# Kernel tuning notes

Hardware: AMD Instinct MI355X
Metric: run time of the kernel (lower is better)

## Reference

```python
import jax, jax.numpy as jnp
import numpy as np

B, S, D = 8, 2048, 2048          # batch, seq, hidden
E, K, NSTEPS = 16, 2, 4          # routed experts, top_k, routers
NSH = 2                          # shared experts
DR = D // 4                      # routed inner dim (routed_ratio=4)
DS = D // 2                      # shared inner dim (shared_ratio=2)


def setup_inputs() -> dict:
    key = jax.random.key(0)
    ks = jax.random.split(key, 8)
    s = 0.02
    return {
        "x": jax.random.normal(ks[0], (B, S, D), jnp.float32),
        "step_t": 1,
        "router_w": jax.random.normal(ks[1], (NSTEPS, D, E), jnp.float32) * s,
        "re_w1": jax.random.normal(ks[2], (E, D, DR), jnp.float32) * s,
        "re_b1": jnp.zeros((E, DR), jnp.float32),
        "re_w2": jax.random.normal(ks[3], (E, DR, D), jnp.float32) * s,
        "re_b2": jnp.zeros((E, D), jnp.float32),
        "sh_w1": jax.random.normal(ks[4], (NSH, D, DS), jnp.float32) * s,
        "sh_b1": jnp.zeros((NSH, DS), jnp.float32),
        "sh_w2": jax.random.normal(ks[5], (NSH, DS, D), jnp.float32) * s,
        "sh_b2": jnp.zeros((NSH, D), jnp.float32),
    }


def reference(x, step_t, router_w, re_w1, re_b1, re_w2, re_b2, sh_w1, sh_b1, sh_w2, sh_b2):
    orig = x.shape
    flat = x.reshape(-1, orig[-1])                       # [T, D]
    T = flat.shape[0]

    # shared expert group: sum of always-active experts
    h = jax.nn.silu(jnp.einsum('td,sdk->tsk', flat, sh_w1) + sh_b1)   # [T, NSH, DS]
    out = jnp.einsum('tsk,skd->td', h, sh_w2) + sh_b2.sum(0)          # [T, D]

    # top-k router for this step (eval mode: no jitter noise)
    logits = flat @ router_w[step_t]                     # [T, E]
    probs = jax.nn.softmax(logits, axis=-1)
    w, idx = jax.lax.top_k(probs, K)                     # [T, K]

    # combine weights per (token, expert): sum_k w_k * 1[idx_k == e]
    cw = jnp.zeros((T, E), flat.dtype).at[jnp.arange(T)[:, None], idx].add(w)

    # routed experts: masked gather-compute-scatter expressed as
    # weighted accumulation (zero combine-weight == token not routed)
    def body(acc, p):
        w1, b1, w2, b2, cwe = p                          # cwe: [T]
        ye = jax.nn.silu(flat @ w1 + b1) @ w2 + b2       # [T, D]
        return acc + cwe[:, None] * ye, None

    out, _ = jax.lax.scan(body, out, (re_w1, re_b1, re_w2, re_b2, cw.T))
    return out.reshape(orig)
```

## Files before the change

kernel.cpp:

```cpp
#include <hip/hip_runtime.h>
#include <hip/hip_bf16.h>
#include <stdint.h>


#define DEV static __device__ __forceinline__

typedef __attribute__((ext_vector_type(8))) short bf16x8;
typedef __attribute__((ext_vector_type(4))) float f32x4;

constexpr int T_TOK = 16384;
constexpr int DIM   = 2048;
constexpr int NEXP  = 16;
constexpr int DR_K  = 512;
constexpr int DS_K  = 1024;
constexpr int MAXROWS = 34816;
constexpr int MAXTILES = 272;

DEV void gload16(const void* g, void* l) {
  __builtin_amdgcn_global_load_lds(
      (const __attribute__((address_space(1))) unsigned int*)g,
      (__attribute__((address_space(3))) unsigned int*)l, 16, 0, 0);
}

DEV float silu_f(float v) { return v / (1.f + __expf(-v)); }

__global__ __launch_bounds__(256) void cast_router_kernel(
    const float* __restrict__ x, __hip_bfloat16* __restrict__ xb,
    const float* __restrict__ rw_all, const int* __restrict__ step_p,
    int* __restrict__ tk_idx, float* __restrict__ tk_w) {
  int tid = threadIdx.x;
  int t0 = blockIdx.x * 8;
  __shared__ float xs[8][1024];
  __shared__ float red[4][4][8][4];

  float acc[8][4];
#pragma unroll
  for (int tk = 0; tk < 8; ++tk)
#pragma unroll
    for (int j = 0; j < 4; ++j) acc[tk][j] = 0.f;

  const float* rwbase = rw_all + (size_t)step_p[0] * DIM * NEXP;

#pragma unroll
  for (int half = 0; half < 2; ++half) {
#pragma unroll
    for (int tk = 0; tk < 8; ++tk) {
      const float4* xp = (const float4*)(x + (size_t)(t0 + tk) * DIM + half * 1024);
      float4 v = xp[tid];
      *(float4*)&xs[tk][tid * 4] = v;
      union { ushort4 u; __hip_bfloat16 h[4]; } o;
      o.h[0] = __float2bfloat16(v.x); o.h[1] = __float2bfloat16(v.y);
      o.h[2] = __float2bfloat16(v.z); o.h[3] = __float2bfloat16(v.w);
      *(ushort4*)(xb + (size_t)(t0 + tk) * DIM + half * 1024 + tid * 4) = o.u;
    }
    __syncthreads();
    const float4* rw4 = (const float4*)(rwbase + (size_t)half * 1024 * NEXP);
#pragma unroll 4
    for (int i = 0; i < 16; ++i) {
      int c = i * 256 + tid;
      int d = c >> 2;
      float4 wv = rw4[c];
#pragma unroll
      for (int tk = 0; tk < 8; ++tk) {
        float v = xs[tk][d];
        acc[tk][0] += v * wv.x; acc[tk][1] += v * wv.y;
        acc[tk][2] += v * wv.z; acc[tk][3] += v * wv.w;
      }
    }
    __syncthreads();
  }

#pragma unroll
  for (int m = 4; m < 64; m <<= 1) {
#pragma unroll
    for (int tk = 0; tk < 8; ++tk) {
      acc[tk][0] += __shfl_xor(acc[tk][0], m);
      acc[tk][1] += __shfl_xor(acc[tk][1], m);
      acc[tk][2] += __shfl_xor(acc[tk][2], m);
      acc[tk][3] += __shfl_xor(acc[tk][3], m);
    }
  }
  int lane = tid & 63, wvi = tid >> 6;
  if (lane < 4) {
#pragma unroll
    for (int tk = 0; tk < 8; ++tk) {
      float4 r = {acc[tk][0], acc[tk][1], acc[tk][2], acc[tk][3]};
      *(float4*)&red[wvi][lane][tk][0] = r;
    }
  }
  __syncthreads();
  if (tid < 8) {
    int t = t0 + tid;
    float lg[16];
#pragma unroll
    for (int e = 0; e < 16; ++e) {
      int cg = e >> 2, j = e & 3;
      lg[e] = red[0][cg][tid][j] + red[1][cg][tid][j] +
              red[2][cg][tid][j] + red[3][cg][tid][j];
    }
    float mx = lg[0];
    for (int i = 1; i < 16; ++i) mx = fmaxf(mx, lg[i]);
    float pr[16], sum = 0.f;
    for (int i = 0; i < 16; ++i) { pr[i] = expf(lg[i] - mx); sum += pr[i]; }
    float inv = 1.f / sum;
    int b0 = -1, b1 = -1; float w0 = -1.f, w1 = -1.f;
    for (int i = 0; i < 16; ++i) {
      float v = pr[i] * inv;
      if (v > w0)      { w1 = w0; b1 = b0; w0 = v; b0 = i; }
      else if (v > w1) { w1 = v; b1 = i; }
    }
    tk_idx[2 * t] = b0; tk_idx[2 * t + 1] = b1;
    tk_w[2 * t] = w0;   tk_w[2 * t + 1] = w1;
  }
}

__global__ __launch_bounds__(256) void hist_kernel(const int* __restrict__ tk_idx,
                                                   int* __restrict__ cnt_pad) {
  __shared__ int lc[16];
  int tid = threadIdx.x;
  if (tid < 16) lc[tid] = 0;
  __syncthreads();
  int base = blockIdx.x * 2048;
#pragma unroll
  for (int i = 0; i < 8; ++i)
    atomicAdd(&lc[tk_idx[base + i * 256 + tid]], 1);
  __syncthreads();
  if (tid < 16) atomicAdd(&cnt_pad[tid * 16], lc[tid]);
}

__global__ __launch_bounds__(256) void transpose_cast(const float* __restrict__ in,
                                                      __hip_bfloat16* __restrict__ out,
                                                      int R, int C) {
  __shared__ float t[64][68];
  size_t bo = (size_t)blockIdx.z * R * C;
  in += bo; out += bo;
  int c0 = blockIdx.x * 64, r0 = blockIdx.y * 64;
  int tid = threadIdx.x;
  int rr = tid >> 2, cc0 = (tid & 3) * 16;
  const float* ip = in + (size_t)(r0 + rr) * C + c0 + cc0;
#pragma unroll
  for (int j = 0; j < 4; ++j)
    *(float4*)&t[rr][cc0 + 4 * j] = *(const float4*)(ip + 4 * j);
  __syncthreads();
  int wr = tid >> 2, wc0 = (tid & 3) * 16;
  union { bf16x8 v; __hip_bfloat16 h[8]; } o0, o1;
#pragma unroll
  for (int k = 0; k < 8; ++k) o0.h[k] = __float2bfloat16(t[wc0 + k][wr]);
#pragma unroll
  for (int k = 0; k < 8; ++k) o1.h[k] = __float2bfloat16(t[wc0 + 8 + k][wr]);
  __hip_bfloat16* op = out + (size_t)(c0 + wr) * R + r0 + wc0;
  *(bf16x8*)op = o0.v;
  *(bf16x8*)(op + 8) = o1.v;
}

__global__ void scan_kernel(const int* __restrict__ cnt_pad, int* __restrict__ seg,
                            int* __restrict__ padded, int* __restrict__ tile_e,
                            int* __restrict__ tile_m0, int* __restrict__ n_tiles) {
  if (threadIdx.x == 0) {
    int off = 0, nt = 0;
    for (int e = 0; e < NEXP; ++e) {
      seg[e] = off;
      int pc = (cnt_pad[e * 16] + 127) & ~127;
      padded[e] = pc;
      for (int m = 0; m < pc; m += 128) { tile_e[nt] = e; tile_m0[nt] = m; ++nt; }
      off += pc;
    }
    seg[NEXP] = off;
    n_tiles[0] = nt;
  }
}

__global__ __launch_bounds__(256) void scatter_kernel(
    const int* __restrict__ tk_idx, const float* __restrict__ tk_w,
    const int* __restrict__ seg, int* __restrict__ cnt2_pad,
    int* __restrict__ tok_list, float* __restrict__ w_list,
    int* __restrict__ pos_list) {
  __shared__ int lh[16], lbase[16];
  int tid = threadIdx.x;
  if (tid < 16) lh[tid] = 0;
  __syncthreads();
  int t = blockIdx.x * 256 + tid;
  int e0 = tk_idx[2 * t], e1 = tk_idx[2 * t + 1];
  int s0 = atomicAdd(&lh[e0], 1);
  int s1 = atomicAdd(&lh[e1], 1);
  __syncthreads();
  if (tid < 16) lbase[tid] = atomicAdd(&cnt2_pad[tid * 16], lh[tid]);
  __syncthreads();
  int p0 = seg[e0] + lbase[e0] + s0;
  int p1 = seg[e1] + lbase[e1] + s1;
  tok_list[p0] = t; w_list[p0] = tk_w[2 * t];     pos_list[2 * t] = p0;
  tok_list[p1] = t; w_list[p1] = tk_w[2 * t + 1]; pos_list[2 * t + 1] = p1;
}

__global__ void pad_kernel(const int* __restrict__ cnt_pad, const int* __restrict__ padded,
                           const int* __restrict__ seg, int* __restrict__ tok_list,
                           float* __restrict__ w_list) {
  int e = blockIdx.x;
  int c = cnt_pad[e * 16], pc = padded[e], s = seg[e];
  for (int i = c + threadIdx.x; i < pc; i += blockDim.x) {
    tok_list[s + i] = 0;
    w_list[s + i] = 0.f;
  }
}

DEV void swz_tile(int bid, int NB, int& tile, int& nb) {
  tile = 8 * (bid / (8 * NB)) + (bid & 7);
  nb = (bid >> 3) % NB;
}

template <int MODE>
DEV void gemm_shared(const __hip_bfloat16* __restrict__ Abase,
                     const __hip_bfloat16* __restrict__ Bt,
                     const float* __restrict__ bias,
                     __hip_bfloat16* __restrict__ outb) {
  constexpr int KD = DIM;
  constexpr int NT = KD / 64;

  int tid = threadIdx.x;
  int ln = tid & 63, w8 = tid >> 6;
  int wm = w8 >> 2, wn = w8 & 3;
  int tile, nb;
  swz_tile(blockIdx.x, 8, tile, nb);
  int m0 = tile * 256;
  int n0 = nb * 256;

  __shared__ __align__(16) char lds[2 * 65536];

  int lrow = w8 * 8 + (ln >> 3);
  int cg8 = (((ln & 7) ^ (ln >> 3)) << 3);
  int browBase;
  if constexpr (MODE == 0) {
    int s = n0 >> 10, nn = n0 & 1023;
    browBase = s * DS_K + nn;
  } else {
    browBase = n0;
  }
  const __hip_bfloat16 *aSrc[2][2], *bSrc[2][2];
  int dA[2][2], dB[2][2];
#pragma unroll
  for (int h = 0; h < 2; ++h)
#pragma unroll
    for (int l = 0; l < 2; ++l) {
      aSrc[h][l] = Abase + (size_t)(m0 + h * 128 + l * 64 + lrow) * KD + cg8;
      bSrc[h][l] = Bt + (size_t)(browBase + h * 128 + l * 64 + lrow) * KD + cg8;
      dA[h][l] = h * 16384 + (l * 8 + w8) * 1024;
      dB[h][l] = 32768 + h * 16384 + (l * 8 + w8) * 1024;
    }

#pragma unroll
  for (int h = 0; h < 2; ++h)
#pragma unroll
    for (int l = 0; l < 2; ++l) {
      gload16(aSrc[h][l], lds + dA[h][l]);
      gload16(bSrc[h][l], lds + dB[h][l]);
    }
  asm volatile("s_waitcnt vmcnt(0)" ::: "memory");
  __builtin_amdgcn_s_barrier();

  f32x4 acc[8][4];
#pragma unroll
  for (int i = 0; i < 8; ++i)
#pragma unroll
    for (int j = 0; j < 4; ++j) acc[i][j] = (f32x4){0.f, 0.f, 0.f, 0.f};

  int rbyte = (ln & 15) * 128;
  int ch0 = (((ln >> 4) ^ (ln & 7)) << 4);
  int ch1 = (((4 + (ln >> 4)) ^ (ln & 7)) << 4);
  int aBase = wm * 16384 + rbyte;
  int bBase = 32768 + wn * 8192 + rbyte;

  bf16x8 af[4][2], bfr[4][2];

  for (int t = 0; t < NT; ++t) {
    const char* buf = lds + (t & 1) * 65536;
    char* nxt = lds + ((t + 1) & 1) * 65536;
    bool pf = (t + 1) < NT;
    int ko = (t + 1) * 64;

    if (pf) {
      gload16(aSrc[0][0] + ko, nxt + dA[0][0]);
      gload16(aSrc[0][1] + ko, nxt + dA[0][1]);
    }
#pragma unroll
    for (int mf = 0; mf < 4; ++mf) {
      af[mf][0] = *(const bf16x8*)(buf + aBase + mf * 2048 + ch0);
      af[mf][1] = *(const bf16x8*)(buf + aBase + mf * 2048 + ch1);
    }
#pragma unroll
    for (int nf = 0; nf < 2; ++nf) {
      bfr[nf][0] = *(const bf16x8*)(buf + bBase + nf * 2048 + ch0);
      bfr[nf][1] = *(const bf16x8*)(buf + bBase + nf * 2048 + ch1);
    }
    __builtin_amdgcn_s_barrier();
    __builtin_amdgcn_s_setprio(1);
#pragma unroll
    for (int mf = 0; mf < 4; ++mf)
#pragma unroll
      for (int nf = 0; nf < 2; ++nf)
#pragma unroll
        for (int kk = 0; kk < 2; ++kk)
          acc[mf][nf] = __builtin_amdgcn_mfma_f32_16x16x32_bf16(
              af[mf][kk], bfr[nf][kk], acc[mf][nf], 0, 0, 0);
    __builtin_amdgcn_s_setprio(0);
    __builtin_amdgcn_s_barrier();

    if (pf) {
      gload16(aSrc[1][0] + ko, nxt + dA[1][0]);
      gload16(aSrc[1][1] + ko, nxt + dA[1][1]);
    }
#pragma unroll
    for (int nf = 2; nf < 4; ++nf) {
      bfr[nf][0] = *(const bf16x8*)(buf + bBase + nf * 2048 + ch0);
      bfr[nf][1] = *(const bf16x8*)(buf + bBase + nf * 2048 + ch1);
    }
    __builtin_amdgcn_s_barrier();
    __builtin_amdgcn_s_setprio(1);
#pragma unroll
    for (int mf = 0; mf < 4; ++mf)
#pragma unroll
      for (int nf = 2; nf < 4; ++nf)
#pragma unroll
        for (int kk = 0; kk < 2; ++kk)
          acc[mf][nf] = __builtin_amdgcn_mfma_f32_16x16x32_bf16(
              af[mf][kk], bfr[nf][kk], acc[mf][nf], 0, 0, 0);
    __builtin_amdgcn_s_setprio(0);
    __builtin_amdgcn_s_barrier();

    if (pf) {
      gload16(bSrc[0][0] + ko, nxt + dB[0][0]);
      gload16(bSrc[0][1] + ko, nxt + dB[0][1]);
    }
#pragma unroll
    for (int mf = 0; mf < 4; ++mf) {
      af[mf][0] = *(const bf16x8*)(buf + aBase + (4 + mf) * 2048 + ch0);
      af[mf][1] = *(const bf16x8*)(buf + aBase + (4 + mf) * 2048 + ch1);
    }
    __builtin_amdgcn_s_barrier();
    __builtin_amdgcn_s_setprio(1);
#pragma unroll
    for (int mf = 0; mf < 4; ++mf)
#pragma unroll
      for (int nf = 0; nf < 2; ++nf)
#pragma unroll
        for (int kk = 0; kk < 2; ++kk)
          acc[4 + mf][nf] = __builtin_amdgcn_mfma_f32_16x16x32_bf16(
              af[mf][kk], bfr[nf][kk], acc[4 + mf][nf], 0, 0, 0);
    __builtin_amdgcn_s_setprio(0);
    __builtin_amdgcn_s_barrier();

    if (pf) {
      gload16(bSrc[1][0] + ko, nxt + dB[1][0]);
      gload16(bSrc[1][1] + ko, nxt + dB[1][1]);
    }
    __builtin_amdgcn_s_setprio(1);
#pragma unroll
    for (int mf = 0; mf < 4; ++mf)
#pragma unroll
      for (int nf = 2; nf < 4; ++nf)
#pragma unroll
        for (int kk = 0; kk < 2; ++kk)
          acc[4 + mf][nf] = __builtin_amdgcn_mfma_f32_16x16x32_bf16(
              af[mf][kk], bfr[nf][kk], acc[4 + mf][nf], 0, 0, 0);
    __builtin_amdgcn_s_setprio(0);

    if (pf) {
      asm volatile("s_waitcnt vmcnt(0)" ::: "memory");
      __builtin_amdgcn_s_barrier();
    }
  }

  int colc = ln & 15;
  int rowb = (ln >> 4) << 2;
#pragma unroll
  for (int mi = 0; mi < 8; ++mi) {
    int mlb = wm * 128 + mi * 16 + rowb;
#pragma unroll
    for (int ni = 0; ni < 4; ++ni) {
      int ng = n0 + wn * 64 + ni * 16 + colc;
#pragma unroll
      for (int j = 0; j < 4; ++j) {
        float v = acc[mi][ni][j];
        if constexpr (MODE == 0) {
          float s = silu_f(v + bias[ng]);
          outb[(size_t)(m0 + mlb + j) * 2048 + ng] = __float2bfloat16(s);
        } else {
          outb[(size_t)(m0 + mlb + j) * DIM + ng] =
              __float2bfloat16(v + bias[ng] + bias[DIM + ng]);
        }
      }
    }
  }
}

template <int MODE, int NB>
DEV void gemm_routed(const __hip_bfloat16* __restrict__ Abase,
                     const __hip_bfloat16* __restrict__ Bt,
                     const float* __restrict__ bias,
                     __hip_bfloat16* __restrict__ outb,
                     const int* __restrict__ tok_list,
                     const float* __restrict__ w_list,
                     const int* __restrict__ seg_off,
                     const int* __restrict__ tile_e,
                     const int* __restrict__ tile_m0,
                     const int* __restrict__ n_tiles) {
  constexpr int KD = (MODE == 3) ? DR_K : DIM;
  constexpr int NT = KD / 32;

  int tid = threadIdx.x;
  int ln = tid & 63, w8 = tid >> 6;
  int wm = w8 >> 2, wn = w8 & 3;

  __shared__ __align__(16) char lds[3 * 24576];
  __shared__ int tk_s[128];
  __shared__ float w_s[128];

  int W = n_tiles[0] * NB;
  int q = (W + 7) >> 3;
  int xcd = blockIdx.x & 7, k = blockIdx.x >> 3;
  if (k >= q) return;
  int w = xcd * q + k;
  if (w >= W) return;
  int tl = w / NB, nb = w % NB;

  int e = tile_e[tl];
  int m0 = tile_m0[tl];
  int n0 = nb * 256;
  int seg = seg_off[e];
  if (tid < 128) {
    if constexpr (MODE == 2) tk_s[tid] = tok_list[seg + m0 + tid];
    w_s[tid] = w_list[seg + m0 + tid];
  }
  __syncthreads();

  int srow = tid >> 2;
  int schunk = (tid & 3) ^ ((tid >> 3) & 3);
  const __hip_bfloat16 *aS, *bS0, *bS1;
  {
    int ar, br0;
    if constexpr (MODE == 2) { ar = tk_s[srow]; br0 = e * DR_K + n0 + srow; }
    else                     { ar = seg + m0 + srow; br0 = e * DIM + n0 + srow; }
    aS  = Abase + (size_t)ar * KD + schunk * 8;
    bS0 = Bt + (size_t)br0 * KD + schunk * 8;
    bS1 = bS0 + (size_t)128 * KD;
  }
  int wlds = w8 * 1024;

#pragma unroll
  for (int tt = 0; tt < 2; ++tt) {
    char* sl = lds + tt * 24576;
    int ko = tt * 32;
    gload16(aS + ko, sl + wlds);
    gload16(bS0 + ko, sl + 8192 + wlds);
    gload16(bS1 + ko, sl + 16384 + wlds);
  }
  asm volatile("s_waitcnt vmcnt(3)" ::: "memory");
  __builtin_amdgcn_s_barrier();

  f32x4 acc[4][4];
#pragma unroll
  for (int i = 0; i < 4; ++i)
#pragma unroll
    for (int j = 0; j < 4; ++j) acc[i][j] = (f32x4){0.f, 0.f, 0.f, 0.f};

  int rof = (ln & 15) * 64 + ((((ln >> 4) ^ (ln >> 1)) & 3) << 4);
  int aoffs = wm * 4096 + rof;
  int boffs = 8192 + wn * 4096 + rof;

  int s0 = 0;
  for (int t = 0; t < NT; ++t) {
    const char* sl = lds + s0 * 24576;
    int sd = s0 - 1; if (sd < 0) sd += 3;
    char* dst = lds + sd * 24576;
    bool pf = (t + 2) < NT;
    int ko = (t + 2) * 32;

    if (pf) {
      gload16(aS + ko, dst + wlds);
      gload16(bS0 + ko, dst + 8192 + wlds);
      gload16(bS1 + ko, dst + 16384 + wlds);
    }
    bf16x8 af[4], bfr[4];
#pragma unroll
    for (int fi = 0; fi < 4; ++fi)
      af[fi] = *(const bf16x8*)(sl + aoffs + fi * 1024);
#pragma unroll
    for (int ni = 0; ni < 4; ++ni)
      bfr[ni] = *(const bf16x8*)(sl + boffs + ni * 1024);
    __builtin_amdgcn_s_barrier();
    __builtin_amdgcn_s_setprio(1);
#pragma unroll
    for (int fi = 0; fi < 4; ++fi)
#pragma unroll
      for (int ni = 0; ni < 4; ++ni)
        acc[fi][ni] = __builtin_amdgcn_mfma_f32_16x16x32_bf16(af[fi], bfr[ni], acc[fi][ni], 0, 0, 0);
    __builtin_amdgcn_s_setprio(0);

    if (t + 1 < NT) {
      if (pf) asm volatile("s_waitcnt vmcnt(3)" ::: "memory");
      else    asm volatile("s_waitcnt vmcnt(0)" ::: "memory");
      __builtin_amdgcn_s_barrier();
    }
    s0 = (s0 + 1 == 3) ? 0 : s0 + 1;
  }

  int colc = ln & 15;
  int rowb = (ln >> 4) << 2;
#pragma unroll
  for (int mi = 0; mi < 4; ++mi) {
    int mlb = wm * 64 + mi * 16 + rowb;
#pragma unroll
    for (int ni = 0; ni < 4; ++ni) {
      int ng = n0 + wn * 64 + ni * 16 + colc;
#pragma unroll
      for (int j = 0; j < 4; ++j) {
        float v = acc[mi][ni][j];
        int ml = mlb + j;
        if constexpr (MODE == 2) {
          float s = silu_f(v + bias[(size_t)e * DR_K + ng]) * w_s[ml];
          outb[((size_t)seg + m0 + ml) * DR_K + ng] = __float2bfloat16(s);
        } else {
          float wv = w_s[ml];
          outb[((size_t)seg + m0 + ml) * DIM + ng] =
              __float2bfloat16(v + wv * bias[(size_t)e * DIM + ng]);
        }
      }
    }
  }
}

__global__ __launch_bounds__(512) void gemm_sh_l1(
    const __hip_bfloat16* A, const __hip_bfloat16* B, const float* bias,
    __hip_bfloat16* ob) {
  gemm_shared<0>(A, B, bias, ob);
}
__global__ __launch_bounds__(512) void gemm_sh_l2(
    const __hip_bfloat16* A, const __hip_bfloat16* B, const float* bias,
    __hip_bfloat16* ob) {
  gemm_shared<1>(A, B, bias, ob);
}
__global__ __launch_bounds__(512) void gemm_re_l1(
    const __hip_bfloat16* A, const __hip_bfloat16* B, const float* bias,
    __hip_bfloat16* ob, const int* tok, const float* wl, const int* seg,
    const int* tl_e, const int* tl_m0, const int* ntl) {
  gemm_routed<2, 2>(A, B, bias, ob, tok, wl, seg, tl_e, tl_m0, ntl);
}
__global__ __launch_bounds__(512) void gemm_re_l2(
    const __hip_bfloat16* A, const __hip_bfloat16* B, const float* bias,
    __hip_bfloat16* ob, const int* tok, const float* wl, const int* seg,
    const int* tl_e, const int* tl_m0, const int* ntl) {
  gemm_routed<3, 8>(A, B, bias, ob, tok, wl, seg, tl_e, tl_m0, ntl);
}

__global__ __launch_bounds__(256) void combine_kernel(float* __restrict__ out,
                                                      const __hip_bfloat16* __restrict__ y_sh,
                                                      const __hip_bfloat16* __restrict__ y_re,
                                                      const int* __restrict__ pos_list) {
  int t = blockIdx.x;
  int d0 = threadIdx.x << 3;
  int p0 = pos_list[2 * t], p1 = pos_list[2 * t + 1];
  union { bf16x8 v; __hip_bfloat16 h[8]; } s, a, b;
  s.v = *(const bf16x8*)(y_sh + (size_t)t * DIM + d0);
  a.v = *(const bf16x8*)(y_re + (size_t)p0 * DIM + d0);
  b.v = *(const bf16x8*)(y_re + (size_t)p1 * DIM + d0);
  float* o = out + (size_t)t * DIM + d0;
  float4 o0, o1;
  o0.x = __bfloat162float(s.h[0]) + __bfloat162float(a.h[0]) + __bfloat162float(b.h[0]);
  o0.y = __bfloat162float(s.h[1]) + __bfloat162float(a.h[1]) + __bfloat162float(b.h[1]);
  o0.z = __bfloat162float(s.h[2]) + __bfloat162float(a.h[2]) + __bfloat162float(b.h[2]);
  o0.w = __bfloat162float(s.h[3]) + __bfloat162float(a.h[3]) + __bfloat162float(b.h[3]);
  o1.x = __bfloat162float(s.h[4]) + __bfloat162float(a.h[4]) + __bfloat162float(b.h[4]);
  o1.y = __bfloat162float(s.h[5]) + __bfloat162float(a.h[5]) + __bfloat162float(b.h[5]);
  o1.z = __bfloat162float(s.h[6]) + __bfloat162float(a.h[6]) + __bfloat162float(b.h[6]);
  o1.w = __bfloat162float(s.h[7]) + __bfloat162float(a.h[7]) + __bfloat162float(b.h[7]);
  *(float4*)o = o0;
  *(float4*)(o + 4) = o1;
}

extern "C" void kernel_launch(void* const* d_in, const int* in_sizes, int n_in,
                              void* d_out, int out_size, void* d_ws, size_t ws_size,
                              hipStream_t stream) {
  const float* x     = (const float*)d_in[0];
  const int* step_p  = (const int*)d_in[1];
  const float* rw    = (const float*)d_in[2];
  const float* re_w1 = (const float*)d_in[3];
  const float* re_b1 = (const float*)d_in[4];
  const float* re_w2 = (const float*)d_in[5];
  const float* re_b2 = (const float*)d_in[6];
  const float* sh_w1 = (const float*)d_in[7];
  const float* sh_b1 = (const float*)d_in[8];
  const float* sh_w2 = (const float*)d_in[9];
  const float* sh_b2 = (const float*)d_in[10];
  float* out = (float*)d_out;

  char* w = (char*)d_ws;
  auto take = [&](size_t bytes) {
    char* p = w;
    w += (bytes + 255) & ~(size_t)255;
    return p;
  };
  __hip_bfloat16* xb     = (__hip_bfloat16*)take((size_t)T_TOK * DIM * 2);
  __hip_bfloat16* h_sh   = (__hip_bfloat16*)take((size_t)T_TOK * 2048 * 2);
  __hip_bfloat16* w1t_sh = (__hip_bfloat16*)take((size_t)2 * DS_K * DIM * 2);
  __hip_bfloat16* w2t_sh = (__hip_bfloat16*)take((size_t)DIM * 2048 * 2);
  __hip_bfloat16* h_re   = (__hip_bfloat16*)take((size_t)MAXROWS * DR_K * 2);
  __hip_bfloat16* w1t_re = (__hip_bfloat16*)take((size_t)NEXP * DR_K * DIM * 2);
  __hip_bfloat16* w2t_re = (__hip_bfloat16*)take((size_t)NEXP * DIM * DR_K * 2);
  __hip_bfloat16* y_sh   = (__hip_bfloat16*)take((size_t)T_TOK * DIM * 2);
  int* tk_idx   = (int*)take((size_t)T_TOK * 2 * 4);
  float* tk_w   = (float*)take((size_t)T_TOK * 2 * 4);
  int* ctrl     = (int*)take(4096);
  int* tok_list = (int*)take((size_t)MAXROWS * 4);
  float* w_list = (float*)take((size_t)MAXROWS * 4);
  int* pos_list = (int*)take((size_t)T_TOK * 2 * 4);
  int* tile_e   = (int*)take((size_t)MAXTILES * 4);
  int* tile_m0  = (int*)take((size_t)MAXTILES * 4);
  int* n_tiles  = (int*)take(256);
  int* cnt_pad  = ctrl;
  int* cnt2_pad = ctrl + 256;
  int* seg      = ctrl + 512;
  int* padded   = ctrl + 544;

  __hip_bfloat16* y_re = (__hip_bfloat16*)d_ws;

  hipMemsetAsync(ctrl, 0, 4096, stream);
  cast_router_kernel<<<T_TOK / 8, 256, 0, stream>>>(x, xb, rw, step_p, tk_idx, tk_w);
  transpose_cast<<<dim3(DS_K / 64, DIM / 64, 2), 256, 0, stream>>>(sh_w1, w1t_sh, DIM, DS_K);
  transpose_cast<<<dim3(DIM / 64, 2048 / 64, 1), 256, 0, stream>>>(sh_w2, w2t_sh, 2048, DIM);
  transpose_cast<<<dim3(DR_K / 64, DIM / 64, NEXP), 256, 0, stream>>>(re_w1, w1t_re, DIM, DR_K);
  transpose_cast<<<dim3(DIM / 64, DR_K / 64, NEXP), 256, 0, stream>>>(re_w2, w2t_re, DR_K, DIM);
  hist_kernel<<<16, 256, 0, stream>>>(tk_idx, cnt_pad);
  scan_kernel<<<1, 32, 0, stream>>>(cnt_pad, seg, padded, tile_e, tile_m0, n_tiles);
  scatter_kernel<<<T_TOK / 256, 256, 0, stream>>>(tk_idx, tk_w, seg, cnt2_pad,
                                                  tok_list, w_list, pos_list);
  pad_kernel<<<NEXP, 256, 0, stream>>>(cnt_pad, padded, seg, tok_list, w_list);

  gemm_sh_l1<<<64 * 8, 512, 0, stream>>>(xb, w1t_sh, sh_b1, h_sh);
  gemm_re_l1<<<MAXTILES * 2, 512, 0, stream>>>(xb, w1t_re, re_b1, h_re,
                                               tok_list, w_list, seg,
                                               tile_e, tile_m0, n_tiles);
  gemm_sh_l2<<<64 * 8, 512, 0, stream>>>(h_sh, w2t_sh, sh_b2, y_sh);
  gemm_re_l2<<<MAXTILES * 8, 512, 0, stream>>>(h_re, w2t_re, re_b2, y_re,
                                               tok_list, w_list, seg,
                                               tile_e, tile_m0, n_tiles);
  combine_kernel<<<T_TOK, 256, 0, stream>>>(out, y_sh, y_re, pos_list);
}
```

Before: 691.7 us.

## Restructure shared-expert GEMM LDS layout into K-halves with partial vmcnt waits

Changes the shared-expert GEMM's LDS staging from a row-major 64-wide K tile to two 32-wide K halves with a new XOR swizzle. The main loop now waits with vmcnt(4) instead of draining all loads, which cuts the per-iteration barriers from about five to two. Loads for the next K half keep streaming while the current half is consumed, hiding global-load latency and reducing synchronisation. The counter-based waits are subtle: if the expected count of in-flight loads is wrong, the kernel can race.

```diff
diff --git a/kernel.cpp b/kernel.cpp
--- a/kernel.cpp
+++ b/kernel.cpp
@@ -226,8 +226,8 @@
 
   __shared__ __align__(16) char lds[2 * 65536];
 
-  int lrow = w8 * 8 + (ln >> 3);
-  int cg8 = (((ln & 7) ^ (ln >> 3)) << 3);
+  int srow = tid >> 2;
+  int schunk = (tid & 3) ^ ((tid >> 3) & 3);
   int browBase;
   if constexpr (MODE == 0) {
     int s = n0 >> 10, nn = n0 & 1023;
@@ -235,27 +235,17 @@
   } else {
     browBase = n0;
   }
-  const __hip_bfloat16 *aSrc[2][2], *bSrc[2][2];
-  int dA[2][2], dB[2][2];
-#pragma unroll
-  for (int h = 0; h < 2; ++h)
-#pragma unroll
-    for (int l = 0; l < 2; ++l) {
-      aSrc[h][l] = Abase + (size_t)(m0 + h * 128 + l * 64 + lrow) * KD + cg8;
-      bSrc[h][l] = Bt + (size_t)(browBase + h * 128 + l * 64 + lrow) * KD + cg8;
-      dA[h][l] = h * 16384 + (l * 8 + w8) * 1024;
-      dB[h][l] = 32768 + h * 16384 + (l * 8 + w8) * 1024;
-    }
-
-#pragma unroll
-  for (int h = 0; h < 2; ++h)
-#pragma unroll
-    for (int l = 0; l < 2; ++l) {
-      gload16(aSrc[h][l], lds + dA[h][l]);
-      gload16(bSrc[h][l], lds + dB[h][l]);
-    }
-  asm volatile("s_waitcnt vmcnt(0)" ::: "memory");
-  __builtin_amdgcn_s_barrier();
+  const __hip_bfloat16* aS0 = Abase + (size_t)(m0 + srow) * KD + schunk * 8;
+  const __hip_bfloat16* aS1 = Abase + (size_t)(m0 + 128 + srow) * KD + schunk * 8;
+  const __hip_bfloat16* bS0 = Bt + (size_t)(browBase + srow) * KD + schunk * 8;
+  const __hip_bfloat16* bS1 = Bt + (size_t)(browBase + 128 + srow) * KD + schunk * 8;
+  int d0 = w8 * 1024;
+  int d1 = 8192 + w8 * 1024;
+
+  gload16(aS0, lds + d0);              gload16(aS1, lds + d1);
+  gload16(bS0, lds + 32768 + d0);      gload16(bS1, lds + 32768 + d1);
+  gload16(aS0 + 32, lds + 16384 + d0); gload16(aS1 + 32, lds + 16384 + d1);
+  gload16(bS0 + 32, lds + 49152 + d0); gload16(bS1 + 32, lds + 49152 + d1);
 
   f32x4 acc[8][4];
 #pragma unroll
@@ -263,13 +253,11 @@
 #pragma unroll
     for (int j = 0; j < 4; ++j) acc[i][j] = (f32x4){0.f, 0.f, 0.f, 0.f};
 
-  int rbyte = (ln & 15) * 128;
-  int ch0 = (((ln >> 4) ^ (ln & 7)) << 4);
-  int ch1 = (((4 + (ln >> 4)) ^ (ln & 7)) << 4);
-  int aBase = wm * 16384 + rbyte;
-  int bBase = 32768 + wn * 8192 + rbyte;
-
-  bf16x8 af[4][2], bfr[4][2];
+  int cswz = (((ln >> 4) ^ ((ln >> 1) & 3)) << 4);
+  int aByte = wm * 8192 + (ln & 15) * 64 + cswz;
+  int bByte = 32768 + wn * 4096 + (ln & 15) * 64 + cswz;
+
+  bf16x8 af[4], bfr[4];
 
   for (int t = 0; t < NT; ++t) {
     const char* buf = lds + (t & 1) * 65536;
@@ -277,96 +265,72 @@
     bool pf = (t + 1) < NT;
     int ko = (t + 1) * 64;
 
+    asm volatile("s_waitcnt vmcnt(4)" ::: "memory");
+    __builtin_amdgcn_s_barrier();
+
     if (pf) {
-      gload16(aSrc[0][0] + ko, nxt + dA[0][0]);
-      gload16(aSrc[0][1] + ko, nxt + dA[0][1]);
-    }
-#pragma unroll
-    for (int mf = 0; mf < 4; ++mf) {
-      af[mf][0] = *(const bf16x8*)(buf + aBase + mf * 2048 + ch0);
-      af[mf][1] = *(const bf16x8*)(buf + aBase + mf * 2048 + ch1);
-    }
-#pragma unroll
-    for (int nf = 0; nf < 2; ++nf) {
-      bfr[nf][0] = *(const bf16x8*)(buf + bBase + nf * 2048 + ch0);
-      bfr[nf][1] = *(const bf16x8*)(buf + bBase + nf * 2048 + ch1);
-    }
+      gload16(aS0 + ko, nxt + d0);
+      gload16(aS1 + ko, nxt + d1);
+    }
+#pragma unroll
+    for (int i = 0; i < 4; ++i) af[i] = *(const bf16x8*)(buf + aByte + i * 1024);
+#pragma unroll
+    for (int n = 0; n < 4; ++n) bfr[n] = *(const bf16x8*)(buf + bByte + n * 1024);
+    __builtin_amdgcn_s_setprio(1);
+#pragma unroll
+    for (int i = 0; i < 4; ++i)
+#pragma unroll
+      for (int n = 0; n < 4; ++n)
+        acc[i][n] = __builtin_amdgcn_mfma_f32_16x16x32_bf16(af[i], bfr[n], acc[i][n], 0, 0, 0);
+    __builtin_amdgcn_s_setprio(0);
+
+    if (pf) {
+      gload16(bS0 + ko, nxt + 32768 + d0);
+      gload16(bS1 + ko, nxt + 32768 + d1);
+    }
+#pragma unroll
+    for (int i = 0; i < 4; ++i) af[i] = *(const bf16x8*)(buf + aByte + (4 + i) * 1024);
+    __builtin_amdgcn_s_setprio(1);
+#pragma unroll
+    for (int i = 0; i < 4; ++i)
+#pragma unroll
+      for (int n = 0; n < 4; ++n)
+        acc[4 + i][n] = __builtin_amdgcn_mfma_f32_16x16x32_bf16(af[i], bfr[n], acc[4 + i][n], 0, 0, 0);
+    __builtin_amdgcn_s_setprio(0);
+
+    if (pf) asm volatile("s_waitcnt vmcnt(4)" ::: "memory");
+    else    asm volatile("s_waitcnt vmcnt(0)" ::: "memory");
     __builtin_amdgcn_s_barrier();
+
+    if (pf) {
+      gload16(aS0 + ko + 32, nxt + 16384 + d0);
+      gload16(aS1 + ko + 32, nxt + 16384 + d1);
+    }
+#pragma unroll
+    for (int i = 0; i < 4; ++i) af[i] = *(const bf16x8*)(buf + 16384 + aByte + i * 1024);
+#pragma unroll
+    for (int n = 0; n < 4; ++n) bfr[n] = *(const bf16x8*)(buf + 16384 + bByte + n * 1024);
     __builtin_amdgcn_s_setprio(1);
 #pragma unroll
-    for (int mf = 0; mf < 4; ++mf)
-#pragma unroll
-      for (int nf = 0; nf < 2; ++nf)
-#pragma unroll
-        for (int kk = 0; kk < 2; ++kk)
-          acc[mf][nf] = __builtin_amdgcn_mfma_f32_16x16x32_bf16(
-              af[mf][kk], bfr[nf][kk], acc[mf][nf], 0, 0, 0);
+    for (int i = 0; i < 4; ++i)
+#pragma unroll
+      for (int n = 0; n < 4; ++n)
+        acc[i][n] = __builtin_amdgcn_mfma_f32_16x16x32_bf16(af[i], bfr[n], acc[i][n], 0, 0, 0);
     __builtin_amdgcn_s_setprio(0);
-    __builtin_amdgcn_s_barrier();
 
     if (pf) {
-      gload16(aSrc[1][0] + ko, nxt + dA[1][0]);
-      gload16(aSrc[1][1] + ko, nxt + dA[1][1]);
-    }
-#pragma unroll
-    for (int nf = 2; nf < 4; ++nf) {
-      bfr[nf][0] = *(const bf16x8*)(buf + bBase + nf * 2048 + ch0);
-      bfr[nf][1] = *(const bf16x8*)(buf + bBase + nf * 2048 + ch1);
-    }
-    __builtin_amdgcn_s_barrier();
+      gload16(bS0 + ko + 32, nxt + 49152 + d0);
+      gload16(bS1 + ko + 32, nxt + 49152 + d1);
+    }
+#pragma unroll
+    for (int i = 0; i < 4; ++i) af[i] = *(const bf16x8*)(buf + 16384 + aByte + (4 + i) * 1024);
     __builtin_amdgcn_s_setprio(1);
 #pragma unroll
-    for (int mf = 0; mf < 4; ++mf)
-#pragma unroll
-      for (int nf = 2; nf < 4; ++nf)
-#pragma unroll
-        for (int kk = 0; kk < 2; ++kk)
-          acc[mf][nf] = __builtin_amdgcn_mfma_f32_16x16x32_bf16(
-              af[mf][kk], bfr[nf][kk], acc[mf][nf], 0, 0, 0);
+    for (int i = 0; i < 4; ++i)
+#pragma unroll
+      for (int n = 0; n < 4; ++n)
+        acc[4 + i][n] = __builtin_amdgcn_mfma_f32_16x16x32_bf16(af[i], bfr[n], acc[4 + i][n], 0, 0, 0);
     __builtin_amdgcn_s_setprio(0);
-    __builtin_amdgcn_s_barrier();
-
-    if (pf) {
-      gload16(bSrc[0][0] + ko, nxt + dB[0][0]);
-      gload16(bSrc[0][1] + ko, nxt + dB[0][1]);
-    }
-#pragma unroll
-    for (int mf = 0; mf < 4; ++mf) {
-      af[mf][0] = *(const bf16x8*)(buf + aBase + (4 + mf) * 2048 + ch0);
-      af[mf][1] = *(const bf16x8*)(buf + aBase + (4 + mf) * 2048 + ch1);
-    }
-    __builtin_amdgcn_s_barrier();
-    __builtin_amdgcn_s_setprio(1);
-#pragma unroll
-    for (int mf = 0; mf < 4; ++mf)
-#pragma unroll
-      for (int nf = 0; nf < 2; ++nf)
-#pragma unroll
-        for (int kk = 0; kk < 2; ++kk)
-          acc[4 + mf][nf] = __builtin_amdgcn_mfma_f32_16x16x32_bf16(
-              af[mf][kk], bfr[nf][kk], acc[4 + mf][nf], 0, 0, 0);
-    __builtin_amdgcn_s_setprio(0);
-    __builtin_amdgcn_s_barrier();
-
-    if (pf) {
-      gload16(bSrc[1][0] + ko, nxt + dB[1][0]);
-      gload16(bSrc[1][1] + ko, nxt + dB[1][1]);
-    }
-    __builtin_amdgcn_s_setprio(1);
-#pragma unroll
-    for (int mf = 0; mf < 4; ++mf)
-#pragma unroll
-      for (int nf = 2; nf < 4; ++nf)
-#pragma unroll
-        for (int kk = 0; kk < 2; ++kk)
-          acc[4 + mf][nf] = __builtin_amdgcn_mfma_f32_16x16x32_bf16(
-              af[mf][kk], bfr[nf][kk], acc[4 + mf][nf], 0, 0, 0);
-    __builtin_amdgcn_s_setprio(0);
-
-    if (pf) {
-      asm volatile("s_waitcnt vmcnt(0)" ::: "memory");
-      __builtin_amdgcn_s_barrier();
-    }
   }
 
   int colc = ln & 15;
```

Result: no change. 686.7 us, median of 3 (-0.7%).
